# Kernel tuning notes

Measured on AMD Instinct MI355X. Metric: run time of the kernel, lower is better.

## Reference

```python
import jax, jax.numpy as jnp
import numpy as np

N_NODES = 50000
N_EDGES = 800000
IN_CH = 128
H = [128, 128, 128]


def _sage_max(x, src, dst, Wl, b, Wr, n_nodes):
    # PyG SAGEConv(aggr='max'): max-aggregate neighbor features, then
    # out = agg @ Wl.T + b + x @ Wr.T ; empty segments -> 0 (torch_scatter).
    agg = jax.ops.segment_max(x[src], dst, num_segments=n_nodes)  # [N, d]
    agg = jnp.where(jnp.isfinite(agg), agg, 0.0)
    return agg @ Wl.T + b + x @ Wr.T


def setup_inputs() -> dict:
    key = jax.random.key(0)
    ks = jax.random.split(key, 24)
    x = jax.random.normal(ks[0], (N_NODES, IN_CH), dtype=jnp.float32)
    edge_index = jax.random.randint(ks[1], (2, N_EDGES), 0, N_NODES, dtype=jnp.int64)
    s = 0.05

    def w(k, o, i):
        return jax.random.normal(k, (o, i), dtype=jnp.float32) * s

    inp = {
        "x": x,
        "edge_index": edge_index,
        "shared_Wl": w(ks[2], H[0], IN_CH), "shared_b": jnp.zeros((H[0],), jnp.float32), "shared_Wr": w(ks[3], H[0], IN_CH),
        "rt1_Wl": w(ks[4], H[1], H[0]), "rt1_b": jnp.zeros((H[1],), jnp.float32), "rt1_Wr": w(ks[5], H[1], H[0]),
        "rt2_Wl": w(ks[6], H[2], H[1]), "rt2_b": jnp.zeros((H[2],), jnp.float32), "rt2_Wr": w(ks[7], H[2], H[1]),
        "rt3_W": w(ks[8], 1, H[2]), "rt3_b": jnp.zeros((1,), jnp.float32),
        "mv1_Wl": w(ks[9], H[1], H[0]), "mv1_b": jnp.zeros((H[1],), jnp.float32), "mv1_Wr": w(ks[10], H[1], H[0]),
        "mv2_Wl": w(ks[11], H[2], H[1]), "mv2_b": jnp.zeros((H[2],), jnp.float32), "mv2_Wr": w(ks[12], H[2], H[1]),
        "mv3_W": w(ks[13], 1, H[2]), "mv3_b": jnp.zeros((1,), jnp.float32),
    }
    return inp


def reference(x, edge_index, shared_Wl, shared_b, shared_Wr,
              rt1_Wl, rt1_b, rt1_Wr, rt2_Wl, rt2_b, rt2_Wr, rt3_W, rt3_b,
              mv1_Wl, mv1_b, mv1_Wr, mv2_Wl, mv2_b, mv2_Wr, mv3_W, mv3_b):
    n = x.shape[0]
    src, dst = edge_index[0], edge_index[1]
    # Eval mode: dropout is identity.
    mv = jax.nn.relu(_sage_max(x, src, dst, shared_Wl, shared_b, shared_Wr, n))

    rt = jax.nn.relu(_sage_max(mv, src, dst, rt1_Wl, rt1_b, rt1_Wr, n))
    rt = jax.nn.relu(_sage_max(rt, src, dst, rt2_Wl, rt2_b, rt2_Wr, n))
    rtAngle = (rt @ rt3_W.T + rt3_b).reshape(-1)

    md = jax.nn.relu(_sage_max(mv, src, dst, mv1_Wl, mv1_b, mv1_Wr, n))
    md = jax.nn.relu(_sage_max(md, src, dst, mv2_Wl, mv2_b, mv2_Wr, n))
    moveDis = (md @ mv3_W.T + mv3_b).reshape(-1)

    return (rtAngle, moveDis)
```

## Files before the change

### kernel.cpp

```cpp
#include <hip/hip_runtime.h>
#include <hip/hip_bf16.h>
#include <hip/hip_fp16.h>
#include <math.h>

#define NN 50000
#define NE 800000
#define C  128
#define NR 8
#define RNG (NN / NR)
typedef unsigned int u32;
typedef unsigned short u16;

using f32x4  = __attribute__((ext_vector_type(4))) float;
using half8  = __attribute__((ext_vector_type(8))) _Float16;
using half2v = __attribute__((ext_vector_type(2))) _Float16;

__device__ __forceinline__ u16 f2h(float f) {
    _Float16 h = (_Float16)f;
    return __builtin_bit_cast(u16, h);
}

__device__ __forceinline__ void gload_lds16(const u16* g, u16* l) {
    __builtin_amdgcn_global_load_lds(
        (const __attribute__((address_space(1))) u32*)g,
        (__attribute__((address_space(3))) u32*)l,
        16, 0, 0);
}


__global__ __launch_bounds__(256) void k_hist_x(const int* __restrict__ dst, int* __restrict__ deg, int nE) {
    int r    = blockIdx.x & (NR - 1);
    int base = (blockIdx.x >> 3) * 4096;
    int lo   = r * RNG, hi = lo + RNG;
    #pragma unroll
    for (int it = 0; it < 16; ++it) {
        int e = base + it * 256 + threadIdx.x;
        if (e < nE) {
            int d = dst[e];
            if (d >= lo && d < hi) atomicAdd(&deg[d], 1);
        }
    }
}

__global__ __launch_bounds__(1024) void k_scan_blk(const int* __restrict__ deg, int* __restrict__ rowptr,
                                                   int* __restrict__ bsum, int n) {
    __shared__ int wsum[16];
    int tid = threadIdx.x, lane = tid & 63, wid = tid >> 6;
    int i = blockIdx.x * 1024 + tid;
    int v = (i < n) ? deg[i] : 0;
    int incl = v;
    #pragma unroll
    for (int d = 1; d < 64; d <<= 1) {
        int t = __shfl_up(incl, d, 64);
        if (lane >= d) incl += t;
    }
    if (lane == 63) wsum[wid] = incl;
    __syncthreads();
    int wo = 0;
    #pragma unroll
    for (int w = 0; w < 16; ++w) wo += (w < wid) ? wsum[w] : 0;
    if (i < n) rowptr[i + 1] = wo + incl;
    if (tid == 1023) bsum[blockIdx.x] = wo + incl;
}

__global__ __launch_bounds__(1024) void k_scan_add(int* __restrict__ rowptr, const int* __restrict__ bsum,
                                                   int n, int nb) {
    __shared__ int soff;
    int tid = threadIdx.x;
    if (tid < 64) {
        int v = (tid < nb) ? bsum[tid] : 0;
        int incl = v;
        #pragma unroll
        for (int d = 1; d < 64; d <<= 1) {
            int t = __shfl_up(incl, d, 64);
            if (tid >= d) incl += t;
        }
        if (tid == blockIdx.x) soff = incl - v;
    }
    __syncthreads();
    int i = blockIdx.x * 1024 + tid;
    if (i == 0) rowptr[0] = 0;
    if (i < n) rowptr[i + 1] += soff;
}

__global__ __launch_bounds__(256) void k_fill_x(const int* __restrict__ src, const int* __restrict__ dst,
                                                const int* __restrict__ rowptr, int* __restrict__ deg,
                                                u16* __restrict__ esrc, int nE) {
    int r    = blockIdx.x & (NR - 1);
    int base = (blockIdx.x >> 3) * 4096;
    int lo   = r * RNG, hi = lo + RNG;
    #pragma unroll
    for (int it = 0; it < 16; ++it) {
        int e = base + it * 256 + threadIdx.x;
        if (e < nE) {
            int d = dst[e];
            if (d >= lo && d < hi) {
                int old = atomicSub(&deg[d], 1);
                esrc[rowptr[d + 1] - old] = (u16)src[e];
            }
        }
    }
}

struct PackArgs {
    const float* Wl[5]; const float* Wr[5];
    u16* Wh[5];
};
__global__ void k_prep(PackArgs pa, const float* __restrict__ x,
                       u32* __restrict__ oh, int* __restrict__ deg, int n64) {
    int bid = blockIdx.x;
    if (bid < 640) {
        int L   = bid >> 7;
        int idx = (bid & 127) * 256 + threadIdx.x;
        int j = idx & 7, l = (idx >> 3) & 63, s = (idx >> 9) & 7, t = idx >> 12;
        int nrow = t * 16 + (l & 15);
        int k    = s * 32 + (l >> 4) * 8 + j;
        float v  = (k < 128) ? pa.Wl[L][nrow * 128 + k] : pa.Wr[L][nrow * 128 + (k - 128)];
        pa.Wh[L][idx] = f2h(v);
    } else {
        int i = (bid - 640) * 256 + threadIdx.x;
        if (i < NN) deg[i] = 0;
        if (i < n64) {
            float2 v = *(const float2*)(x + (size_t)i * 2);
            oh[i] = ((u32)f2h(v.x)) | (((u32)f2h(v.y)) << 16);
        }
    }
}


__global__ __launch_bounds__(256) void k_segmax_h(const u32* __restrict__ h2, const int* __restrict__ rowptr,
                                                  const u16* __restrict__ esrc, u32* __restrict__ agg2, int n) {
    int node = blockIdx.x * 4 + (threadIdx.x >> 6);
    int lane = threadIdx.x & 63;
    if (node >= n) return;
    int beg = rowptr[node], end = rowptr[node + 1];
    _Float16 ninf = (_Float16)(-INFINITY);
    half2v m = {ninf, ninf};
    int last = end - 1;
    for (int i = beg; i < end; i += 16) {
        u32 w[16];
        #pragma unroll
        for (int q = 0; q < 16; ++q) {
            int e = i + q; if (e > last) e = last;
            w[q] = h2[((size_t)esrc[e] << 6) + lane];
        }
        #pragma unroll
        for (int q = 0; q < 16; ++q)
            m = __builtin_elementwise_max(m, __builtin_bit_cast(half2v, w[q]));
    }
    u32 r = (end > beg) ? __builtin_bit_cast(u32, m) : 0u;
    __builtin_nontemporal_store(r, &agg2[(size_t)node * 64 + lane]);
}

__global__ __launch_bounds__(256) void k_segmax_h2s(const u32* __restrict__ hA, const u32* __restrict__ hB,
                                                    const int* __restrict__ rowptr, const u16* __restrict__ esrc,
                                                    u32* __restrict__ aggA, u32* __restrict__ aggB, int n) {
    int pl   = blockIdx.x & 1;
    int node = (blockIdx.x >> 1) * 4 + (threadIdx.x >> 6);
    int lane = threadIdx.x & 63;
    if (node >= n) return;
    const u32* h2 = pl ? hB : hA;
    u32* agg2     = pl ? aggB : aggA;
    int beg = rowptr[node], end = rowptr[node + 1];
    _Float16 ninf = (_Float16)(-INFINITY);
    half2v m = {ninf, ninf};
    int last = end - 1;
    for (int i = beg; i < end; i += 16) {
        u32 w[16];
        #pragma unroll
        for (int q = 0; q < 16; ++q) {
            int e = i + q; if (e > last) e = last;
            w[q] = h2[((size_t)esrc[e] << 6) + lane];
        }
        #pragma unroll
        for (int q = 0; q < 16; ++q)
            m = __builtin_elementwise_max(m, __builtin_bit_cast(half2v, w[q]));
    }
    u32 r = (end > beg) ? __builtin_bit_cast(u32, m) : 0u;
    __builtin_nontemporal_store(r, &agg2[(size_t)node * 64 + lane]);
}

template<int HEAD>
__device__ __forceinline__ void gemm_body(
        const u16* __restrict__ Ahi, const u16* __restrict__ Xh,
        const u16* __restrict__ Wh, const float* __restrict__ bias,
        u32* __restrict__ outh,
        const float* __restrict__ hw, const float* __restrict__ hb,
        float* __restrict__ hout, int n, int bid, u16 (*smw)[4096]) {
    int tid  = threadIdx.x;
    int wave = tid >> 6, lane = tid & 63;
    int rit  = lane & 15, kgrp = lane >> 4;
    int m0   = bid * 128 + wave * 32;
    int ar0  = m0 + rit;      if (ar0 > n - 1) ar0 = n - 1;
    int ar1  = m0 + 16 + rit; if (ar1 > n - 1) ar1 = n - 1;

    #define STAGEH(s_, b_) do {                                                  \
        _Pragma("unroll")                                                        \
        for (int q = 0; q < 2; ++q) {                                            \
            int tt = wave * 2 + q;                                               \
            const u16* g = Wh + (((tt << 3) + (s_)) << 9) + (lane << 3);         \
            gload_lds16(g, &smw[b_][tt << 9]);                                   \
        }                                                                        \
    } while (0)

    half8 a0[4], a1[4], xh0[4], xh1[4];
    #pragma unroll
    for (int s = 0; s < 4; ++s) {
        size_t o0 = (size_t)ar0 * C + s * 32 + kgrp * 8;
        size_t o1 = (size_t)ar1 * C + s * 32 + kgrp * 8;
        a0[s]  = *(const half8*)(Ahi + o0);
        a1[s]  = *(const half8*)(Ahi + o1);
        xh0[s] = *(const half8*)(Xh + o0);
        xh1[s] = *(const half8*)(Xh + o1);
    }

    f32x4 acc0[8], acc1[8];
    #pragma unroll
    for (int t = 0; t < 8; ++t) {
        acc0[t] = (f32x4){0.f, 0.f, 0.f, 0.f};
        acc1[t] = (f32x4){0.f, 0.f, 0.f, 0.f};
    }

    STAGEH(0, 0);
    __syncthreads();

    #pragma unroll
    for (int s = 0; s < 8; ++s) {
        if (s < 7) STAGEH(s + 1, (s + 1) & 1);
        const u16* base = smw[s & 1];
        half8 f0 = (s < 4) ? a0[s] : xh0[s - 4];
        half8 f1 = (s < 4) ? a1[s] : xh1[s - 4];
        #pragma unroll
        for (int t = 0; t < 8; ++t) {
            half8 wv = *(const half8*)(base + (t << 9) + (lane << 3));
            acc0[t] = __builtin_amdgcn_mfma_f32_16x16x32_f16(f0, wv, acc0[t], 0, 0, 0);
            acc1[t] = __builtin_amdgcn_mfma_f32_16x16x32_f16(f1, wv, acc1[t], 0, 0, 0);
        }
        if (s < 7) __syncthreads();
    }
    #undef STAGEH

    if (HEAD) {
        float hsA[4] = {0.f, 0.f, 0.f, 0.f}, hsB[4] = {0.f, 0.f, 0.f, 0.f};
        #pragma unroll
        for (int t = 0; t < 8; ++t) {
            int col = t * 16 + rit;
            float b = bias[col], w = hw[col];
            #pragma unroll
            for (int j = 0; j < 4; ++j) {
                hsA[j] += fmaxf(acc0[t][j] + b, 0.f) * w;
                hsB[j] += fmaxf(acc1[t][j] + b, 0.f) * w;
            }
        }
        #pragma unroll
        for (int msk = 1; msk < 16; msk <<= 1) {
            #pragma unroll
            for (int j = 0; j < 4; ++j) {
                hsA[j] += __shfl_xor(hsA[j], msk, 64);
                hsB[j] += __shfl_xor(hsB[j], msk, 64);
            }
        }
        if (rit == 0) {
            float hbv = hb[0];
            #pragma unroll
            for (int j = 0; j < 4; ++j) {
                int rA = m0 + kgrp * 4 + j;
                int rB = rA + 16;
                if (rA < n) hout[rA] = hsA[j] + hbv;
                if (rB < n) hout[rB] = hsB[j] + hbv;
            }
        }
    } else {
        #pragma unroll
        for (int g = 0; g < 2; ++g) {
            int rbase = m0 + g * 16 + kgrp * 4;
            #pragma unroll
            for (int t = 0; t < 8; ++t) {
                int col = t * 16 + rit;
                float b = bias[col];
                #pragma unroll
                for (int j = 0; j < 4; ++j) {
                    int rr = rbase + j;
                    float v = fmaxf((g ? acc1[t][j] : acc0[t][j]) + b, 0.f);
                    float pv = __shfl_xor(v, 1, 64);
                    if (!(rit & 1) && rr < n)
                        outh[(size_t)rr * 64 + (col >> 1)] = ((u32)f2h(v)) | (((u32)f2h(pv)) << 16);
                }
            }
        }
    }
}

__global__ __launch_bounds__(256, 2) void k_gemm_p(
        const u16* __restrict__ Ahi, const u16* __restrict__ Xh,
        const u16* __restrict__ Wh, const float* __restrict__ bias, u32* __restrict__ outh, int n) {
    __shared__ __align__(16) u16 smw[2][4096];
    gemm_body<0>(Ahi, Xh, Wh, bias, outh, nullptr, nullptr, nullptr, n, blockIdx.x, smw);
}

__global__ __launch_bounds__(256, 2) void k_gemm_heads(
        const u16* __restrict__ AhiA, const u16* __restrict__ XhA,
        const u16* __restrict__ WhA, const float* __restrict__ biasA,
        const float* __restrict__ hwA, const float* __restrict__ hbA, float* __restrict__ houtA,
        const u16* __restrict__ AhiB, const u16* __restrict__ XhB,
        const u16* __restrict__ WhB, const float* __restrict__ biasB,
        const float* __restrict__ hwB, const float* __restrict__ hbB, float* __restrict__ houtB,
        int n) {
    __shared__ __align__(16) u16 smw[2][4096];
    int br  = blockIdx.x & 1;
    int bid = blockIdx.x >> 1;
    gemm_body<1>(br ? AhiB : AhiA, br ? XhB : XhA, br ? WhB : WhA,
                 br ? biasB : biasA, nullptr,
                 br ? hwB : hwA, br ? hbB : hbA, br ? houtB : houtA,
                 n, bid, smw);
}

__global__ __launch_bounds__(256, 2) void k_gemm_p2(
        const u16* __restrict__ Ahi, const u16* __restrict__ Xh,
        const u16* __restrict__ Wh1, const float* __restrict__ b1, u32* __restrict__ out1,
        const u16* __restrict__ Wh2, const float* __restrict__ b2, u32* __restrict__ out2, int n) {
    __shared__ __align__(16) u16 smw[2][8192];
    int tid  = threadIdx.x;
    int wave = tid >> 6, lane = tid & 63;
    int rit  = lane & 15, kgrp = lane >> 4;
    int m0   = blockIdx.x * 128 + wave * 32;
    int ar0  = m0 + rit;      if (ar0 > n - 1) ar0 = n - 1;
    int ar1  = m0 + 16 + rit; if (ar1 > n - 1) ar1 = n - 1;

    #define STAGE2H(s_, b_) do {                                                 \
        _Pragma("unroll")                                                        \
        for (int q = 0; q < 4; ++q) {                                            \
            int kk = wave * 4 + q;                                               \
            int set = kk >> 3, tt = kk & 7;                                      \
            const u16* g = (set ? Wh2 : Wh1) + (((tt << 3) + (s_)) << 9) + (lane << 3); \
            gload_lds16(g, &smw[b_][set * 4096 + (tt << 9)]);                    \
        }                                                                        \
    } while (0)

    half8 a0[4], a1[4], xh0[4], xh1[4];
    #pragma unroll
    for (int s = 0; s < 4; ++s) {
        size_t o0 = (size_t)ar0 * C + s * 32 + kgrp * 8;
        size_t o1 = (size_t)ar1 * C + s * 32 + kgrp * 8;
        a0[s]  = *(const half8*)(Ahi + o0);
        a1[s]  = *(const half8*)(Ahi + o1);
        xh0[s] = *(const half8*)(Xh + o0);
        xh1[s] = *(const half8*)(Xh + o1);
    }

    f32x4 accA0[8], accA1[8], accB0[8], accB1[8];
    #pragma unroll
    for (int t = 0; t < 8; ++t) {
        accA0[t] = (f32x4){0.f, 0.f, 0.f, 0.f};
        accA1[t] = (f32x4){0.f, 0.f, 0.f, 0.f};
        accB0[t] = (f32x4){0.f, 0.f, 0.f, 0.f};
        accB1[t] = (f32x4){0.f, 0.f, 0.f, 0.f};
    }

    STAGE2H(0, 0);
    __syncthreads();

    #pragma unroll
    for (int s = 0; s < 8; ++s) {
        if (s < 7) STAGE2H(s + 1, (s + 1) & 1);
        const u16* base = smw[s & 1];
        half8 f0 = (s < 4) ? a0[s] : xh0[s - 4];
        half8 f1 = (s < 4) ? a1[s] : xh1[s - 4];
        #pragma unroll
        for (int t = 0; t < 8; ++t) {
            half8 wa = *(const half8*)(base + (t << 9) + (lane << 3));
            half8 wb = *(const half8*)(base + 4096 + (t << 9) + (lane << 3));
            accA0[t] = __builtin_amdgcn_mfma_f32_16x16x32_f16(f0, wa, accA0[t], 0, 0, 0);
            accA1[t] = __builtin_amdgcn_mfma_f32_16x16x32_f16(f1, wa, accA1[t], 0, 0, 0);
            accB0[t] = __builtin_amdgcn_mfma_f32_16x16x32_f16(f0, wb, accB0[t], 0, 0, 0);
            accB1[t] = __builtin_amdgcn_mfma_f32_16x16x32_f16(f1, wb, accB1[t], 0, 0, 0);
        }
        if (s < 7) __syncthreads();
    }
    #undef STAGE2H

    #pragma unroll
    for (int e = 0; e < 2; ++e) {
        const float* bb = e ? b2 : b1;
        u32* oo = e ? out2 : out1;
        #pragma unroll
        for (int g = 0; g < 2; ++g) {
            int rbase = m0 + g * 16 + kgrp * 4;
            #pragma unroll
            for (int t = 0; t < 8; ++t) {
                int col = t * 16 + rit;
                float b = bb[col];
                #pragma unroll
                for (int j = 0; j < 4; ++j) {
                    int rr = rbase + j;
                    float acv = e ? (g ? accB1[t][j] : accB0[t][j])
                                  : (g ? accA1[t][j] : accA0[t][j]);
                    float v = fmaxf(acv + b, 0.f);
                    float pv = __shfl_xor(v, 1, 64);
                    if (!(rit & 1) && rr < n)
                        oo[(size_t)rr * 64 + (col >> 1)] = ((u32)f2h(v)) | (((u32)f2h(pv)) << 16);
                }
            }
        }
    }
}


extern "C" void kernel_launch(void* const* d_in, const int* in_sizes, int n_in,
                              void* d_out, int out_size, void* d_ws, size_t ws_size,
                              hipStream_t stream) {
    const float* x     = (const float*)d_in[0];
    const int*   ei    = (const int*)d_in[1];
    const int*   src   = ei;
    const int*   dstp  = ei + NE;
    const float* sWl   = (const float*)d_in[2];
    const float* sB    = (const float*)d_in[3];
    const float* sWr   = (const float*)d_in[4];
    const float* rt1Wl = (const float*)d_in[5];
    const float* rt1B  = (const float*)d_in[6];
    const float* rt1Wr = (const float*)d_in[7];
    const float* rt2Wl = (const float*)d_in[8];
    const float* rt2B  = (const float*)d_in[9];
    const float* rt2Wr = (const float*)d_in[10];
    const float* rt3W  = (const float*)d_in[11];
    const float* rt3B  = (const float*)d_in[12];
    const float* mv1Wl = (const float*)d_in[13];
    const float* mv1B  = (const float*)d_in[14];
    const float* mv1Wr = (const float*)d_in[15];
    const float* mv2Wl = (const float*)d_in[16];
    const float* mv2B  = (const float*)d_in[17];
    const float* mv2Wr = (const float*)d_in[18];
    const float* mv3W  = (const float*)d_in[19];
    const float* mv3B  = (const float*)d_in[20];
    float* out = (float*)d_out;

    char* ws = (char*)d_ws;
    int* rowptr  = (int*)ws;
    int* deg     = rowptr + (NN + 1);
    int* bsum    = deg + NN;
    u16* esrc16  = (u16*)(bsum + 64);
    size_t off   = (((size_t)(NN + 1 + NN + 64) * 4 + (size_t)NE * 2) + 255) & ~(size_t)255;
    u32* P[5];
    for (int i = 0; i < 5; ++i) P[i] = (u32*)(ws + off) + (size_t)i * NN * 64;
    u16* wpack = (u16*)(P[4] + (size_t)NN * 64);
    u16* pk[5];
    for (int L = 0; L < 5; ++L) pk[L] = wpack + (size_t)L * 32768;

    const int NB = (NN + 1023) / 1024;
    const int GCH = ((NE + 4095) / 4096) * NR;
    const int NCVT = (NN * 64 + 255) / 256;

    PackArgs pa;
    pa.Wl[0] = sWl;   pa.Wr[0] = sWr;
    pa.Wl[1] = rt1Wl; pa.Wr[1] = rt1Wr;
    pa.Wl[2] = rt2Wl; pa.Wr[2] = rt2Wr;
    pa.Wl[3] = mv1Wl; pa.Wr[3] = mv1Wr;
    pa.Wl[4] = mv2Wl; pa.Wr[4] = mv2Wr;
    for (int L = 0; L < 5; ++L) pa.Wh[L] = pk[L];
    k_prep<<<640 + NCVT, 256, 0, stream>>>(pa, x, P[0], deg, NN * 64);

    k_hist_x<<<GCH, 256, 0, stream>>>(dstp, deg, NE);
    k_scan_blk<<<NB, 1024, 0, stream>>>(deg, rowptr, bsum, NN);
    k_scan_add<<<NB, 1024, 0, stream>>>(rowptr, bsum, NN, NB);
    k_fill_x<<<GCH, 256, 0, stream>>>(src, dstp, rowptr, deg, esrc16, NE);

    dim3 gSeg((NN + 3) / 4), bSeg(256);
    const int GT = (NN + 127) / 128;

    k_segmax_h<<<gSeg, bSeg, 0, stream>>>(P[0], rowptr, esrc16, P[1], NN);
    k_gemm_p<<<GT, 256, 0, stream>>>((const u16*)P[1], (const u16*)P[0],
                                     pk[0], sB, P[2], NN);
    k_segmax_h<<<gSeg, bSeg, 0, stream>>>(P[2], rowptr, esrc16, P[3], NN);
    k_gemm_p2<<<GT, 256, 0, stream>>>((const u16*)P[3], (const u16*)P[2],
                                      pk[1], rt1B, P[1],
                                      pk[3], mv1B, P[4], NN);
    k_segmax_h2s<<<dim3(2 * ((NN + 3) / 4)), bSeg, 0, stream>>>(
        P[1], P[4], rowptr, esrc16, P[0], P[3], NN);
    k_gemm_heads<<<2 * GT, 256, 0, stream>>>(
        (const u16*)P[0], (const u16*)P[1], pk[2], rt2B, rt3W, rt3B, out,
        (const u16*)P[3], (const u16*)P[4], pk[4], mv2B, mv3W, mv3B, out + NN,
        NN);
}
```

Baseline: 251.3 us.

## Split segment-max across column quarters with four edge slots per wave

The segment-max kernels now split each node's 64 half2 columns into four quarter blocks. Each wave handles one quarter, with four 16-lane slots walking different edges in parallel, followed by a cross-slot shuffle-max reduction. This trades per-lane sequential edge iteration and clamped tail loads for more blocks and narrower 64-byte row gathers. The aim is more memory-level parallelism and less wasted tail work at an average degree of about 16, at the cost of four times as many blocks and extra shuffles.

```diff
diff --git a/kernel.cpp b/kernel.cpp
--- a/kernel.cpp
+++ b/kernel.cpp
@@ -127,57 +127,65 @@
     }
 }
 
-
-__global__ __launch_bounds__(256) void k_segmax_h(const u32* __restrict__ h2, const int* __restrict__ rowptr,
-                                                  const u16* __restrict__ esrc, u32* __restrict__ agg2, int n) {
-    int node = blockIdx.x * 4 + (threadIdx.x >> 6);
+__device__ __forceinline__ void segq_body(const u32* __restrict__ h2, const int* __restrict__ rowptr,
+                                          const u16* __restrict__ esrc, u32* __restrict__ agg2,
+                                          int node, int q, int n) {
+    if (node >= n) return;
     int lane = threadIdx.x & 63;
-    if (node >= n) return;
+    int slot = lane >> 4, cl = lane & 15;
     int beg = rowptr[node], end = rowptr[node + 1];
+    int last = end - 1;
     _Float16 ninf = (_Float16)(-INFINITY);
     half2v m = {ninf, ninf};
-    int last = end - 1;
-    for (int i = beg; i < end; i += 16) {
-        u32 w[16];
-        #pragma unroll
-        for (int q = 0; q < 16; ++q) {
-            int e = i + q; if (e > last) e = last;
-            w[q] = h2[((size_t)esrc[e] << 6) + lane];
-        }
-        #pragma unroll
-        for (int q = 0; q < 16; ++q)
-            m = __builtin_elementwise_max(m, __builtin_bit_cast(half2v, w[q]));
-    }
-    u32 r = (end > beg) ? __builtin_bit_cast(u32, m) : 0u;
-    __builtin_nontemporal_store(r, &agg2[(size_t)node * 64 + lane]);
-}
-
-__global__ __launch_bounds__(256) void k_segmax_h2s(const u32* __restrict__ hA, const u32* __restrict__ hB,
-                                                    const int* __restrict__ rowptr, const u16* __restrict__ esrc,
-                                                    u32* __restrict__ aggA, u32* __restrict__ aggB, int n) {
-    int pl   = blockIdx.x & 1;
-    int node = (blockIdx.x >> 1) * 4 + (threadIdx.x >> 6);
-    int lane = threadIdx.x & 63;
-    if (node >= n) return;
-    const u32* h2 = pl ? hB : hA;
-    u32* agg2     = pl ? aggB : aggA;
-    int beg = rowptr[node], end = rowptr[node + 1];
-    _Float16 ninf = (_Float16)(-INFINITY);
-    half2v m = {ninf, ninf};
-    int last = end - 1;
-    for (int i = beg; i < end; i += 16) {
-        u32 w[16];
-        #pragma unroll
-        for (int q = 0; q < 16; ++q) {
-            int e = i + q; if (e > last) e = last;
-            w[q] = h2[((size_t)esrc[e] << 6) + lane];
-        }
-        #pragma unroll
-        for (int q = 0; q < 16; ++q)
-            m = __builtin_elementwise_max(m, __builtin_bit_cast(half2v, w[q]));
-    }
-    u32 r = (end > beg) ? __builtin_bit_cast(u32, m) : 0u;
-    __builtin_nontemporal_store(r, &agg2[(size_t)node * 64 + lane]);
+    int qoff = (q << 4) + cl;
+    int i = beg;
+    for (; i + 16 <= end; i += 16) {
+        u32 w[4];
+        #pragma unroll
+        for (int g = 0; g < 4; ++g)
+            w[g] = h2[((size_t)esrc[i + g * 4 + slot] << 6) + qoff];
+        #pragma unroll
+        for (int g = 0; g < 4; ++g)
+            m = __builtin_elementwise_max(m, __builtin_bit_cast(half2v, w[g]));
+    }
+    if (i < end) {
+        u32 w[4];
+        #pragma unroll
+        for (int g = 0; g < 4; ++g) {
+            int e = i + g * 4 + slot; if (e > last) e = last;
+            w[g] = h2[((size_t)esrc[e] << 6) + qoff];
+        }
+        #pragma unroll
+        for (int g = 0; g < 4; ++g)
+            m = __builtin_elementwise_max(m, __builtin_bit_cast(half2v, w[g]));
+    }
+    u32 mm = __builtin_bit_cast(u32, m);
+    u32 t1 = __shfl_xor(mm, 16, 64);
+    half2v m2 = __builtin_elementwise_max(__builtin_bit_cast(half2v, mm),
+                                          __builtin_bit_cast(half2v, t1));
+    mm = __builtin_bit_cast(u32, m2);
+    u32 t2 = __shfl_xor(mm, 32, 64);
+    m2 = __builtin_elementwise_max(__builtin_bit_cast(half2v, mm),
+                                   __builtin_bit_cast(half2v, t2));
+    u32 r = (end > beg) ? __builtin_bit_cast(u32, m2) : 0u;
+    if (slot == 0)
+        __builtin_nontemporal_store(r, &agg2[(size_t)node * 64 + qoff]);
+}
+
+__global__ __launch_bounds__(256) void k_segmax_q(const u32* __restrict__ h2, const int* __restrict__ rowptr,
+                                                  const u16* __restrict__ esrc, u32* __restrict__ agg2, int n) {
+    int q    = blockIdx.x & 3;
+    int node = (blockIdx.x >> 2) * 4 + (threadIdx.x >> 6);
+    segq_body(h2, rowptr, esrc, agg2, node, q, n);
+}
+
+__global__ __launch_bounds__(256) void k_segmax_q2(const u32* __restrict__ hA, const u32* __restrict__ hB,
+                                                   const int* __restrict__ rowptr, const u16* __restrict__ esrc,
+                                                   u32* __restrict__ aggA, u32* __restrict__ aggB, int n) {
+    int combo = blockIdx.x & 7;
+    int pl = combo & 1, q = combo >> 1;
+    int node = (blockIdx.x >> 3) * 4 + (threadIdx.x >> 6);
+    segq_body(pl ? hB : hA, rowptr, esrc, pl ? aggB : aggA, node, q, n);
 }
 
 template<int HEAD>
@@ -464,17 +472,17 @@
     k_scan_add<<<NB, 1024, 0, stream>>>(rowptr, bsum, NN, NB);
     k_fill_x<<<GCH, 256, 0, stream>>>(src, dstp, rowptr, deg, esrc16, NE);
 
-    dim3 gSeg((NN + 3) / 4), bSeg(256);
     const int GT = (NN + 127) / 128;
-
-    k_segmax_h<<<gSeg, bSeg, 0, stream>>>(P[0], rowptr, esrc16, P[1], NN);
+    const int GS = (NN + 3) / 4;
+
+    k_segmax_q<<<dim3(GS * 4), 256, 0, stream>>>(P[0], rowptr, esrc16, P[1], NN);
     k_gemm_p<<<GT, 256, 0, stream>>>((const u16*)P[1], (const u16*)P[0],
                                      pk[0], sB, P[2], NN);
-    k_segmax_h<<<gSeg, bSeg, 0, stream>>>(P[2], rowptr, esrc16, P[3], NN);
+    k_segmax_q<<<dim3(GS * 4), 256, 0, stream>>>(P[2], rowptr, esrc16, P[3], NN);
     k_gemm_p2<<<GT, 256, 0, stream>>>((const u16*)P[3], (const u16*)P[2],
                                       pk[1], rt1B, P[1],
                                       pk[3], mv1B, P[4], NN);
-    k_segmax_h2s<<<dim3(2 * ((NN + 3) / 4)), bSeg, 0, stream>>>(
+    k_segmax_q2<<<dim3(GS * 8), 256, 0, stream>>>(
         P[1], P[4], rowptr, esrc16, P[0], P[3], NN);
     k_gemm_heads<<<2 * GT, 256, 0, stream>>>(
         (const u16*)P[0], (const u16*)P[1], pk[2], rt2B, rt3W, rt3B, out,
```

Measured after the change: 362.1 us. 44.1% more time.

## Process two nodes per wave in segment-max and fuse histogram into prep kernel

Applied to the files above, without the earlier changes.

Each segment-max wave now handles two destination nodes and interleaves their gather loads, so more independent memory requests are in flight per wave and there are half as many blocks. Row bounds are made wave-uniform with readfirstlane. Separately, the degree histogram is merged into the weight-pack and feature-convert kernel, and a small zeroing kernel is added beforehand, which trades one launch for another. Nodes with very different degrees paired in one wave leave lanes idle, and the extra register arrays may lower occupancy.

```diff
diff --git a/kernel.cpp b/kernel.cpp
--- a/kernel.cpp
+++ b/kernel.cpp
@@ -8,6 +8,7 @@
 #define C  128
 #define NR 8
 #define RNG (NN / NR)
+#define GCH 1568
 typedef unsigned int u32;
 typedef unsigned short u16;
 
@@ -28,16 +29,44 @@
 }
 
 
-__global__ __launch_bounds__(256) void k_hist_x(const int* __restrict__ dst, int* __restrict__ deg, int nE) {
-    int r    = blockIdx.x & (NR - 1);
-    int base = (blockIdx.x >> 3) * 4096;
-    int lo   = r * RNG, hi = lo + RNG;
-    #pragma unroll
-    for (int it = 0; it < 16; ++it) {
-        int e = base + it * 256 + threadIdx.x;
-        if (e < nE) {
-            int d = dst[e];
-            if (d >= lo && d < hi) atomicAdd(&deg[d], 1);
+__global__ __launch_bounds__(1024) void k_zero(int* __restrict__ p, int n) {
+    int i = blockIdx.x * 1024 + threadIdx.x;
+    if (i < n) p[i] = 0;
+}
+
+struct PackArgs {
+    const float* Wl[5]; const float* Wr[5];
+    u16* Wh[5];
+};
+__global__ void k_preph(PackArgs pa, const float* __restrict__ x, u32* __restrict__ oh,
+                        const int* __restrict__ dst, int* __restrict__ deg, int n64, int nE) {
+    int bid = blockIdx.x;
+    if (bid < GCH) {
+        int r    = bid & (NR - 1);
+        int base = (bid >> 3) * 4096;
+        int lo   = r * RNG, hi = lo + RNG;
+        #pragma unroll
+        for (int it = 0; it < 16; ++it) {
+            int e = base + it * 256 + threadIdx.x;
+            if (e < nE) {
+                int d = dst[e];
+                if (d >= lo && d < hi) atomicAdd(&deg[d], 1);
+            }
+        }
+    } else if (bid < GCH + 640) {
+        int b   = bid - GCH;
+        int L   = b >> 7;
+        int idx = (b & 127) * 256 + threadIdx.x;
+        int j = idx & 7, l = (idx >> 3) & 63, s = (idx >> 9) & 7, t = idx >> 12;
+        int nrow = t * 16 + (l & 15);
+        int k    = s * 32 + (l >> 4) * 8 + j;
+        float v  = (k < 128) ? pa.Wl[L][nrow * 128 + k] : pa.Wr[L][nrow * 128 + (k - 128)];
+        pa.Wh[L][idx] = f2h(v);
+    } else {
+        int i = (bid - GCH - 640) * 256 + threadIdx.x;
+        if (i < n64) {
+            float2 v = *(const float2*)(x + (size_t)i * 2);
+            oh[i] = ((u32)f2h(v.x)) | (((u32)f2h(v.y)) << 16);
         }
     }
 }
@@ -102,82 +131,79 @@
     }
 }
 
-struct PackArgs {
-    const float* Wl[5]; const float* Wr[5];
-    u16* Wh[5];
-};
-__global__ void k_prep(PackArgs pa, const float* __restrict__ x,
-                       u32* __restrict__ oh, int* __restrict__ deg, int n64) {
-    int bid = blockIdx.x;
-    if (bid < 640) {
-        int L   = bid >> 7;
-        int idx = (bid & 127) * 256 + threadIdx.x;
-        int j = idx & 7, l = (idx >> 3) & 63, s = (idx >> 9) & 7, t = idx >> 12;
-        int nrow = t * 16 + (l & 15);
-        int k    = s * 32 + (l >> 4) * 8 + j;
-        float v  = (k < 128) ? pa.Wl[L][nrow * 128 + k] : pa.Wr[L][nrow * 128 + (k - 128)];
-        pa.Wh[L][idx] = f2h(v);
-    } else {
-        int i = (bid - 640) * 256 + threadIdx.x;
-        if (i < NN) deg[i] = 0;
-        if (i < n64) {
-            float2 v = *(const float2*)(x + (size_t)i * 2);
-            oh[i] = ((u32)f2h(v.x)) | (((u32)f2h(v.y)) << 16);
-        }
-    }
-}
-
+__device__ __forceinline__ void seg2_body(const u32* __restrict__ h2, const int* __restrict__ rowptr,
+                                          const u16* __restrict__ esrc, u32* __restrict__ agg2,
+                                          int node0, int node1, int lane, int n) {
+    int beg0 = 0, end0 = 0, beg1 = 0, end1 = 0;
+    if (node0 < n) {
+        beg0 = __builtin_amdgcn_readfirstlane(rowptr[node0]);
+        end0 = __builtin_amdgcn_readfirstlane(rowptr[node0 + 1]);
+    }
+    if (node1 < n) {
+        beg1 = __builtin_amdgcn_readfirstlane(rowptr[node1]);
+        end1 = __builtin_amdgcn_readfirstlane(rowptr[node1 + 1]);
+    }
+    _Float16 ninf = (_Float16)(-INFINITY);
+    half2v m0 = {ninf, ninf}, m1 = {ninf, ninf};
+    int i0 = beg0, i1 = beg1;
+    int last0 = end0 - 1, last1 = end1 - 1;
+    while ((i0 < end0) || (i1 < end1)) {
+        u32 w0[16], w1[16];
+        bool a0 = i0 < end0, a1 = i1 < end1;
+        if (a0) {
+            #pragma unroll
+            for (int q = 0; q < 16; ++q) {
+                int e = i0 + q; if (e > last0) e = last0;
+                w0[q] = h2[((size_t)esrc[e] << 6) + lane];
+            }
+        }
+        if (a1) {
+            #pragma unroll
+            for (int q = 0; q < 16; ++q) {
+                int e = i1 + q; if (e > last1) e = last1;
+                w1[q] = h2[((size_t)esrc[e] << 6) + lane];
+            }
+        }
+        if (a0) {
+            #pragma unroll
+            for (int q = 0; q < 16; ++q)
+                m0 = __builtin_elementwise_max(m0, __builtin_bit_cast(half2v, w0[q]));
+            i0 += 16;
+        }
+        if (a1) {
+            #pragma unroll
+            for (int q = 0; q < 16; ++q)
+                m1 = __builtin_elementwise_max(m1, __builtin_bit_cast(half2v, w1[q]));
+            i1 += 16;
+        }
+    }
+    if (node0 < n) {
+        u32 r = (end0 > beg0) ? __builtin_bit_cast(u32, m0) : 0u;
+        __builtin_nontemporal_store(r, &agg2[(size_t)node0 * 64 + lane]);
+    }
+    if (node1 < n) {
+        u32 r = (end1 > beg1) ? __builtin_bit_cast(u32, m1) : 0u;
+        __builtin_nontemporal_store(r, &agg2[(size_t)node1 * 64 + lane]);
+    }
+}
 
 __global__ __launch_bounds__(256) void k_segmax_h(const u32* __restrict__ h2, const int* __restrict__ rowptr,
                                                   const u16* __restrict__ esrc, u32* __restrict__ agg2, int n) {
-    int node = blockIdx.x * 4 + (threadIdx.x >> 6);
-    int lane = threadIdx.x & 63;
-    if (node >= n) return;
-    int beg = rowptr[node], end = rowptr[node + 1];
-    _Float16 ninf = (_Float16)(-INFINITY);
-    half2v m = {ninf, ninf};
-    int last = end - 1;
-    for (int i = beg; i < end; i += 16) {
-        u32 w[16];
-        #pragma unroll
-        for (int q = 0; q < 16; ++q) {
-            int e = i + q; if (e > last) e = last;
-            w[q] = h2[((size_t)esrc[e] << 6) + lane];
-        }
-        #pragma unroll
-        for (int q = 0; q < 16; ++q)
-            m = __builtin_elementwise_max(m, __builtin_bit_cast(half2v, w[q]));
-    }
-    u32 r = (end > beg) ? __builtin_bit_cast(u32, m) : 0u;
-    __builtin_nontemporal_store(r, &agg2[(size_t)node * 64 + lane]);
+    int w = threadIdx.x >> 6, lane = threadIdx.x & 63;
+    int node0 = blockIdx.x * 8 + w;
+    int node1 = node0 + 4;
+    seg2_body(h2, rowptr, esrc, agg2, node0, node1, lane, n);
 }
 
 __global__ __launch_bounds__(256) void k_segmax_h2s(const u32* __restrict__ hA, const u32* __restrict__ hB,
                                                     const int* __restrict__ rowptr, const u16* __restrict__ esrc,
                                                     u32* __restrict__ aggA, u32* __restrict__ aggB, int n) {
-    int pl   = blockIdx.x & 1;
-    int node = (blockIdx.x >> 1) * 4 + (threadIdx.x >> 6);
-    int lane = threadIdx.x & 63;
-    if (node >= n) return;
-    const u32* h2 = pl ? hB : hA;
-    u32* agg2     = pl ? aggB : aggA;
-    int beg = rowptr[node], end = rowptr[node + 1];
-    _Float16 ninf = (_Float16)(-INFINITY);
-    half2v m = {ninf, ninf};
-    int last = end - 1;
-    for (int i = beg; i < end; i += 16) {
-        u32 w[16];
-        #pragma unroll
-        for (int q = 0; q < 16; ++q) {
-            int e = i + q; if (e > last) e = last;
-            w[q] = h2[((size_t)esrc[e] << 6) + lane];
-        }
-        #pragma unroll
-        for (int q = 0; q < 16; ++q)
-            m = __builtin_elementwise_max(m, __builtin_bit_cast(half2v, w[q]));
-    }
-    u32 r = (end > beg) ? __builtin_bit_cast(u32, m) : 0u;
-    __builtin_nontemporal_store(r, &agg2[(size_t)node * 64 + lane]);
+    int pl = blockIdx.x & 1;
+    int nb = blockIdx.x >> 1;
+    int w = threadIdx.x >> 6, lane = threadIdx.x & 63;
+    int node0 = nb * 8 + w;
+    int node1 = node0 + 4;
+    seg2_body(pl ? hB : hA, rowptr, esrc, pl ? aggB : aggA, node0, node1, lane, n);
 }
 
 template<int HEAD>
@@ -447,7 +473,6 @@
     for (int L = 0; L < 5; ++L) pk[L] = wpack + (size_t)L * 32768;
 
     const int NB = (NN + 1023) / 1024;
-    const int GCH = ((NE + 4095) / 4096) * NR;
     const int NCVT = (NN * 64 + 255) / 256;
 
     PackArgs pa;
@@ -457,24 +482,24 @@
     pa.Wl[3] = mv1Wl; pa.Wr[3] = mv1Wr;
     pa.Wl[4] = mv2Wl; pa.Wr[4] = mv2Wr;
     for (int L = 0; L < 5; ++L) pa.Wh[L] = pk[L];
-    k_prep<<<640 + NCVT, 256, 0, stream>>>(pa, x, P[0], deg, NN * 64);
-
-    k_hist_x<<<GCH, 256, 0, stream>>>(dstp, deg, NE);
+
+    k_zero<<<NB, 1024, 0, stream>>>(deg, NN);
+    k_preph<<<GCH + 640 + NCVT, 256, 0, stream>>>(pa, x, P[0], dstp, deg, NN * 64, NE);
     k_scan_blk<<<NB, 1024, 0, stream>>>(deg, rowptr, bsum, NN);
     k_scan_add<<<NB, 1024, 0, stream>>>(rowptr, bsum, NN, NB);
     k_fill_x<<<GCH, 256, 0, stream>>>(src, dstp, rowptr, deg, esrc16, NE);
 
-    dim3 gSeg((NN + 3) / 4), bSeg(256);
     const int GT = (NN + 127) / 128;
-
-    k_segmax_h<<<gSeg, bSeg, 0, stream>>>(P[0], rowptr, esrc16, P[1], NN);
+    const int GS8 = (NN + 7) / 8;
+
+    k_segmax_h<<<GS8, 256, 0, stream>>>(P[0], rowptr, esrc16, P[1], NN);
     k_gemm_p<<<GT, 256, 0, stream>>>((const u16*)P[1], (const u16*)P[0],
                                      pk[0], sB, P[2], NN);
-    k_segmax_h<<<gSeg, bSeg, 0, stream>>>(P[2], rowptr, esrc16, P[3], NN);
+    k_segmax_h<<<GS8, 256, 0, stream>>>(P[2], rowptr, esrc16, P[3], NN);
     k_gemm_p2<<<GT, 256, 0, stream>>>((const u16*)P[3], (const u16*)P[2],
                                       pk[1], rt1B, P[1],
                                       pk[3], mv1B, P[4], NN);
-    k_segmax_h2s<<<dim3(2 * ((NN + 3) / 4)), bSeg, 0, stream>>>(
+    k_segmax_h2s<<<2 * GS8, 256, 0, stream>>>(
         P[1], P[4], rowptr, esrc16, P[0], P[3], NN);
     k_gemm_heads<<<2 * GT, 256, 0, stream>>>(
         (const u16*)P[0], (const u16*)P[1], pk[2], rt2B, rt3W, rt3B, out,
```

New measurement: 251.9 us. Within noise of the previous version (+0.2%).
